# Optimization experiments

Hardware: AMD Instinct MI355X
Metric: run time of the kernel (lower is better)

The kernel has to match this reference:

```python
import jax, jax.numpy as jnp
import numpy as np

N = 8192       # number of points
C = 16         # num_colors (size of color distribution)
DIM = 2        # spatial dim (GeometricLoss(dim=2))


def setup_inputs() -> dict:
    key = jax.random.key(0)
    k1, k2 = jax.random.split(key)
    outputs = jax.random.normal(k1, (N, C), dtype=jnp.float32)
    points = jax.random.normal(k2, (N, DIM), dtype=jnp.float32)
    return {"outputs": outputs, "points": points, "k": 5}


def reference(outputs, points, k):
    # cdist(points, points) via the squared-norm expansion (avoids [N,N,dim] tensor)
    sq = jnp.sum(points * points, axis=1)                      # [N]
    d2 = sq[:, None] + sq[None, :] - 2.0 * (points @ points.T)  # [N,N]
    dist = jnp.sqrt(jnp.maximum(d2, 0.0))
    # k+1 smallest distances per row; drop self (distance 0)
    _, idx = jax.lax.top_k(-dist, k + 1)                        # [N,k+1]
    idx = idx[:, 1:]                                            # [N,k]
    neighbor_outputs = outputs[idx]                             # [N,k,C] gather
    # ||out_i - out_j|| over color dim, mean over all (i, neighbor) pairs
    differences = jnp.linalg.norm(outputs[:, None, :] - neighbor_outputs, axis=2)
    return differences.mean()
```

## Files before the change

### kernel.cpp

```cpp
#include <hip/hip_runtime.h>


static constexpr int NPTS  = 8192;
static constexpr int KNN   = 5;
static constexpr int CH    = 16;
static constexpr int WPB   = 4;
static constexpr int QPW   = 4;
static constexpr int NWAVE = NPTS / QPW;
static constexpr int NBLK  = NWAVE / WPB;
static constexpr int CAP   = 128;
static constexpr int NF4   = NPTS / 2;
static constexpr int BAT   = 4;
static constexpr int NIT   = NF4 / 64;
static constexpr int NB    = NIT / BAT;

__device__ __forceinline__ unsigned long long shfl_xor_u64(unsigned long long v, int m) {
    unsigned int lo = (unsigned int)v;
    unsigned int hi = (unsigned int)(v >> 32);
    lo = __shfl_xor(lo, m, 64);
    hi = __shfl_xor(hi, m, 64);
    return ((unsigned long long)hi << 32) | lo;
}

__global__ __launch_bounds__(256, 4) void knn_loss_kernel(
        const float* __restrict__ outputs,
        const float* __restrict__ points,
        float* __restrict__ partial) {
    const int wave  = threadIdx.x >> 6;
    const int lane  = threadIdx.x & 63;
    const int w     = blockIdx.x * WPB + wave;
    const int qbase = w * QPW;

    const float2* __restrict__ pts2 = (const float2*)points;
    const float4* __restrict__ pts4 = (const float4*)points;
    const float FINF = __int_as_float(0x7f800000);

    float pix[QPW], piy[QPW];
    #pragma unroll
    for (int q = 0; q < QPW; ++q) {
        const float2 p = pts2[qbase + q];
        pix[q] = p.x; piy[q] = p.y;
    }

    float acc[QPW];
    #pragma unroll
    for (int q = 0; q < QPW; ++q) acc[q] = FINF;

    for (int b = 0; b < NB; ++b) {
        float4 p[BAT];
        #pragma unroll
        for (int u = 0; u < BAT; ++u)
            p[u] = pts4[b * (BAT * 64) + u * 64 + lane];
        #pragma unroll
        for (int u = 0; u < BAT; ++u) {
            #pragma unroll
            for (int q = 0; q < QPW; ++q) {
                const float dxa = pix[q] - p[u].x, dya = piy[q] - p[u].y;
                const float dxb = pix[q] - p[u].z, dyb = piy[q] - p[u].w;
                const float d2a = fmaf(dxa, dxa, dya * dya);
                const float d2b = fmaf(dxb, dxb, dyb * dyb);
                acc[q] = fminf(fminf(acc[q], d2a), d2b);
            }
        }
    }

    float v[QPW], T[QPW];
    #pragma unroll
    for (int q = 0; q < QPW; ++q) v[q] = fmaxf(acc[q], 0.0f);
    #pragma unroll
    for (int t = 0; t < KNN + 1; ++t) {
        float m[QPW];
        #pragma unroll
        for (int q = 0; q < QPW; ++q) m[q] = v[q];
        #pragma unroll
        for (int d = 1; d < 64; d <<= 1) {
            #pragma unroll
            for (int q = 0; q < QPW; ++q)
                m[q] = fminf(m[q], __shfl_xor(m[q], d, 64));
        }
        #pragma unroll
        for (int q = 0; q < QPW; ++q) {
            if (v[q] == m[q]) v[q] = FINF;
            T[q] = m[q];
        }
    }

    __shared__ unsigned long long buf[WPB][QPW][CAP];
    __shared__ int cnt[WPB][QPW];
    __shared__ float red[WPB];
    if (lane < QPW) cnt[wave][lane] = 0;
    __syncthreads();

    for (int b = 0; b < NB; ++b) {
        float4 p[BAT];
        #pragma unroll
        for (int u = 0; u < BAT; ++u)
            p[u] = pts4[b * (BAT * 64) + u * 64 + lane];
        #pragma unroll
        for (int u = 0; u < BAT; ++u) {
            const int it = b * (BAT * 64) + u * 64 + lane;
            #pragma unroll
            for (int q = 0; q < QPW; ++q) {
                const float dxa = pix[q] - p[u].x, dya = piy[q] - p[u].y;
                const float dxb = pix[q] - p[u].z, dyb = piy[q] - p[u].w;
                const float d2a = fmaf(dxa, dxa, dya * dya);
                const float d2b = fmaf(dxb, dxb, dyb * dyb);
                if (d2a <= T[q] || d2b <= T[q]) {
                    if (d2a <= T[q]) {
                        const int pos = atomicAdd(&cnt[wave][q], 1);
                        if (pos < CAP)
                            buf[wave][q][pos] =
                                ((unsigned long long)__float_as_uint(fmaxf(d2a, 0.0f)) << 32)
                                | (unsigned int)(2 * it);
                    }
                    if (d2b <= T[q]) {
                        const int pos = atomicAdd(&cnt[wave][q], 1);
                        if (pos < CAP)
                            buf[wave][q][pos] =
                                ((unsigned long long)__float_as_uint(fmaxf(d2b, 0.0f)) << 32)
                                | (unsigned int)(2 * it + 1);
                    }
                }
            }
        }
    }
    __syncthreads();

    const unsigned long long INF64 = ~0ull;
    unsigned int myj = 0;
    int myi = 0, active = 0;
    #pragma unroll
    for (int q = 0; q < QPW; ++q) {
        const int n = min(cnt[wave][q], CAP);
        unsigned long long a  = (lane      < n) ? buf[wave][q][lane]      : INF64;
        unsigned long long b2 = (lane + 64 < n) ? buf[wave][q][lane + 64] : INF64;
        if (b2 < a) { unsigned long long t = a; a = b2; b2 = t; }
        #pragma unroll
        for (int t = 0; t < KNN + 1; ++t) {
            unsigned long long m = a;
            #pragma unroll
            for (int d = 1; d < 64; d <<= 1) {
                const unsigned long long x = shfl_xor_u64(m, d);
                if (x < m) m = x;
            }
            if (a == m) { a = b2; b2 = INF64; }
            if (t >= 1 && lane == q * 8 + t) {
                myj = (unsigned int)m; myi = qbase + q; active = 1;
            }
        }
    }

    float nrm = 0.0f;
    if (active) {
        const float4* oi = (const float4*)(outputs + (size_t)myi * CH);
        const float4* oj = (const float4*)(outputs + (size_t)myj * CH);
        float s = 0.0f;
        #pragma unroll
        for (int c = 0; c < 4; ++c) {
            const float4 x = oi[c], y = oj[c];
            const float dx = x.x - y.x, dy = x.y - y.y;
            const float dz = x.z - y.z, dw = x.w - y.w;
            s += dx * dx + dy * dy + dz * dz + dw * dw;
        }
        nrm = sqrtf(s);
    }
    #pragma unroll
    for (int d = 1; d < 64; d <<= 1) nrm += __shfl_xor(nrm, d, 64);

    if (lane == 0) red[wave] = nrm;
    __syncthreads();
    if (threadIdx.x == 0)
        partial[blockIdx.x] = red[0] + red[1] + red[2] + red[3];
}

__global__ __launch_bounds__(256) void finalize_kernel(
        const float* __restrict__ partial, float* __restrict__ out) {
    double s = 0.0;
    for (int idx = threadIdx.x; idx < NBLK; idx += 256) s += (double)partial[idx];
    #pragma unroll
    for (int d = 1; d < 64; d <<= 1) s += __shfl_xor(s, d, 64);
    __shared__ double lds[4];
    const int wave = threadIdx.x >> 6;
    const int lane = threadIdx.x & 63;
    if (lane == 0) lds[wave] = s;
    __syncthreads();
    if (threadIdx.x == 0)
        out[0] = (float)((lds[0] + lds[1] + lds[2] + lds[3]) /
                         (double)((long long)NPTS * KNN));
}

extern "C" void kernel_launch(void* const* d_in, const int* in_sizes, int n_in,
                              void* d_out, int out_size, void* d_ws, size_t ws_size,
                              hipStream_t stream) {
    const float* outputs = (const float*)d_in[0];
    const float* points  = (const float*)d_in[1];
    float* partial = (float*)d_ws;
    float* out = (float*)d_out;

    knn_loss_kernel<<<NBLK, 256, 0, stream>>>(outputs, points, partial);
    finalize_kernel<<<1, 256, 0, stream>>>(partial, out);
}
```

Baseline: 93.52 us.

## Split each query's candidate scan across a whole block instead of one wave

```diff
diff --git a/kernel.cpp b/kernel.cpp
--- a/kernel.cpp
+++ b/kernel.cpp
@@ -1,18 +1,17 @@
 #include <hip/hip_runtime.h>
 
 
-static constexpr int NPTS  = 8192;
-static constexpr int KNN   = 5;
-static constexpr int CH    = 16;
-static constexpr int WPB   = 4;
-static constexpr int QPW   = 4;
-static constexpr int NWAVE = NPTS / QPW;
-static constexpr int NBLK  = NWAVE / WPB;
-static constexpr int CAP   = 128;
-static constexpr int NF4   = NPTS / 2;
-static constexpr int BAT   = 4;
-static constexpr int NIT   = NF4 / 64;
-static constexpr int NB    = NIT / BAT;
+static constexpr int NPTS    = 8192;
+static constexpr int KNN     = 5;
+static constexpr int CH      = 16;
+static constexpr int QPB     = 4;
+static constexpr int THREADS = 256;
+static constexpr int NBLK    = NPTS / QPB;
+static constexpr int CAP     = 128;
+static constexpr int NF4     = NPTS / 2;
+static constexpr int ITERS   = NF4 / THREADS;
+static constexpr int BAT     = 4;
+static constexpr int NB      = ITERS / BAT;
 
 __device__ __forceinline__ unsigned long long shfl_xor_u64(unsigned long long v, int m) {
     unsigned int lo = (unsigned int)v;
@@ -22,39 +21,39 @@
     return ((unsigned long long)hi << 32) | lo;
 }
 
-__global__ __launch_bounds__(256, 4) void knn_loss_kernel(
+__global__ __launch_bounds__(256, 8) void knn_loss_kernel(
         const float* __restrict__ outputs,
         const float* __restrict__ points,
         float* __restrict__ partial) {
-    const int wave  = threadIdx.x >> 6;
-    const int lane  = threadIdx.x & 63;
-    const int w     = blockIdx.x * WPB + wave;
-    const int qbase = w * QPW;
+    const int tid  = threadIdx.x;
+    const int wave = tid >> 6;
+    const int lane = tid & 63;
+    const int qbase = blockIdx.x * QPB;
 
     const float2* __restrict__ pts2 = (const float2*)points;
     const float4* __restrict__ pts4 = (const float4*)points;
     const float FINF = __int_as_float(0x7f800000);
 
-    float pix[QPW], piy[QPW];
-    #pragma unroll
-    for (int q = 0; q < QPW; ++q) {
+    float pix[QPB], piy[QPB];
+    #pragma unroll
+    for (int q = 0; q < QPB; ++q) {
         const float2 p = pts2[qbase + q];
         pix[q] = p.x; piy[q] = p.y;
     }
 
-    float acc[QPW];
-    #pragma unroll
-    for (int q = 0; q < QPW; ++q) acc[q] = FINF;
+    float acc[QPB];
+    #pragma unroll
+    for (int q = 0; q < QPB; ++q) acc[q] = FINF;
 
     for (int b = 0; b < NB; ++b) {
         float4 p[BAT];
         #pragma unroll
         for (int u = 0; u < BAT; ++u)
-            p[u] = pts4[b * (BAT * 64) + u * 64 + lane];
+            p[u] = pts4[b * (BAT * THREADS) + u * THREADS + tid];
         #pragma unroll
         for (int u = 0; u < BAT; ++u) {
             #pragma unroll
-            for (int q = 0; q < QPW; ++q) {
+            for (int q = 0; q < QPB; ++q) {
                 const float dxa = pix[q] - p[u].x, dya = piy[q] - p[u].y;
                 const float dxb = pix[q] - p[u].z, dyb = piy[q] - p[u].w;
                 const float d2a = fmaf(dxa, dxa, dya * dya);
@@ -64,59 +63,73 @@
         }
     }
 
-    float v[QPW], T[QPW];
-    #pragma unroll
-    for (int q = 0; q < QPW; ++q) v[q] = fmaxf(acc[q], 0.0f);
-    #pragma unroll
-    for (int t = 0; t < KNN + 1; ++t) {
-        float m[QPW];
-        #pragma unroll
-        for (int q = 0; q < QPW; ++q) m[q] = v[q];
-        #pragma unroll
-        for (int d = 1; d < 64; d <<= 1) {
+    __shared__ float thrmin[QPB][THREADS];
+    __shared__ unsigned long long buf[QPB][CAP];
+    __shared__ int cnt[QPB];
+    __shared__ float Ts[QPB];
+    __shared__ float red[QPB];
+
+    #pragma unroll
+    for (int q = 0; q < QPB; ++q)
+        thrmin[q][tid] = fmaxf(acc[q], 0.0f);
+    if (tid < QPB) cnt[tid] = 0;
+    __syncthreads();
+
+    {
+        const float4 tv = ((const float4*)thrmin[wave])[lane];
+        float v = fminf(fminf(tv.x, tv.y), fminf(tv.z, tv.w));
+        float T = 0.0f;
+        #pragma unroll
+        for (int t = 0; t < KNN + 1; ++t) {
+            float m = v;
             #pragma unroll
-            for (int q = 0; q < QPW; ++q)
-                m[q] = fminf(m[q], __shfl_xor(m[q], d, 64));
-        }
-        #pragma unroll
-        for (int q = 0; q < QPW; ++q) {
-            if (v[q] == m[q]) v[q] = FINF;
-            T[q] = m[q];
-        }
-    }
-
-    __shared__ unsigned long long buf[WPB][QPW][CAP];
-    __shared__ int cnt[WPB][QPW];
-    __shared__ float red[WPB];
-    if (lane < QPW) cnt[wave][lane] = 0;
-    __syncthreads();
+            for (int d = 1; d < 64; d <<= 1) m = fminf(m, __shfl_xor(m, d, 64));
+            if (v == m) v = FINF;
+            T = m;
+        }
+        if (lane == 0) Ts[wave] = T;
+    }
+    __syncthreads();
+
+    float Tq[QPB];
+    #pragma unroll
+    for (int q = 0; q < QPB; ++q) Tq[q] = Ts[q];
 
     for (int b = 0; b < NB; ++b) {
         float4 p[BAT];
         #pragma unroll
         for (int u = 0; u < BAT; ++u)
-            p[u] = pts4[b * (BAT * 64) + u * 64 + lane];
+            p[u] = pts4[b * (BAT * THREADS) + u * THREADS + tid];
         #pragma unroll
         for (int u = 0; u < BAT; ++u) {
-            const int it = b * (BAT * 64) + u * 64 + lane;
+            const int it = b * (BAT * THREADS) + u * THREADS + tid;
+            float g = FINF;
             #pragma unroll
-            for (int q = 0; q < QPW; ++q) {
+            for (int q = 0; q < QPB; ++q) {
                 const float dxa = pix[q] - p[u].x, dya = piy[q] - p[u].y;
                 const float dxb = pix[q] - p[u].z, dyb = piy[q] - p[u].w;
                 const float d2a = fmaf(dxa, dxa, dya * dya);
                 const float d2b = fmaf(dxb, dxb, dyb * dyb);
-                if (d2a <= T[q] || d2b <= T[q]) {
-                    if (d2a <= T[q]) {
-                        const int pos = atomicAdd(&cnt[wave][q], 1);
+                g = fminf(g, fminf(d2a, d2b) - Tq[q]);
+            }
+            if (g <= 0.0f) {
+                #pragma unroll
+                for (int q = 0; q < QPB; ++q) {
+                    const float dxa = pix[q] - p[u].x, dya = piy[q] - p[u].y;
+                    const float dxb = pix[q] - p[u].z, dyb = piy[q] - p[u].w;
+                    const float d2a = fmaf(dxa, dxa, dya * dya);
+                    const float d2b = fmaf(dxb, dxb, dyb * dyb);
+                    if (d2a <= Tq[q]) {
+                        const int pos = atomicAdd(&cnt[q], 1);
                         if (pos < CAP)
-                            buf[wave][q][pos] =
+                            buf[q][pos] =
                                 ((unsigned long long)__float_as_uint(fmaxf(d2a, 0.0f)) << 32)
                                 | (unsigned int)(2 * it);
                     }
-                    if (d2b <= T[q]) {
-                        const int pos = atomicAdd(&cnt[wave][q], 1);
+                    if (d2b <= Tq[q]) {
+                        const int pos = atomicAdd(&cnt[q], 1);
                         if (pos < CAP)
-                            buf[wave][q][pos] =
+                            buf[q][pos] =
                                 ((unsigned long long)__float_as_uint(fmaxf(d2b, 0.0f)) << 32)
                                 | (unsigned int)(2 * it + 1);
                     }
@@ -127,32 +140,28 @@
     __syncthreads();
 
     const unsigned long long INF64 = ~0ull;
+    const int n = min(cnt[wave], CAP);
+    unsigned long long a  = (lane      < n) ? buf[wave][lane]      : INF64;
+    unsigned long long b2 = (lane + 64 < n) ? buf[wave][lane + 64] : INF64;
+    if (b2 < a) { unsigned long long t = a; a = b2; b2 = t; }
+
     unsigned int myj = 0;
-    int myi = 0, active = 0;
-    #pragma unroll
-    for (int q = 0; q < QPW; ++q) {
-        const int n = min(cnt[wave][q], CAP);
-        unsigned long long a  = (lane      < n) ? buf[wave][q][lane]      : INF64;
-        unsigned long long b2 = (lane + 64 < n) ? buf[wave][q][lane + 64] : INF64;
-        if (b2 < a) { unsigned long long t = a; a = b2; b2 = t; }
-        #pragma unroll
-        for (int t = 0; t < KNN + 1; ++t) {
-            unsigned long long m = a;
-            #pragma unroll
-            for (int d = 1; d < 64; d <<= 1) {
-                const unsigned long long x = shfl_xor_u64(m, d);
-                if (x < m) m = x;
-            }
-            if (a == m) { a = b2; b2 = INF64; }
-            if (t >= 1 && lane == q * 8 + t) {
-                myj = (unsigned int)m; myi = qbase + q; active = 1;
-            }
-        }
+    int active = 0;
+    #pragma unroll
+    for (int t = 0; t < KNN + 1; ++t) {
+        unsigned long long m = a;
+        #pragma unroll
+        for (int d = 1; d < 64; d <<= 1) {
+            const unsigned long long x = shfl_xor_u64(m, d);
+            if (x < m) m = x;
+        }
+        if (a == m) { a = b2; b2 = INF64; }
+        if (t >= 1 && lane == t) { myj = (unsigned int)m; active = 1; }
     }
 
     float nrm = 0.0f;
     if (active) {
-        const float4* oi = (const float4*)(outputs + (size_t)myi * CH);
+        const float4* oi = (const float4*)(outputs + (size_t)(qbase + wave) * CH);
         const float4* oj = (const float4*)(outputs + (size_t)myj * CH);
         float s = 0.0f;
         #pragma unroll
@@ -169,7 +178,7 @@
 
     if (lane == 0) red[wave] = nrm;
     __syncthreads();
-    if (threadIdx.x == 0)
+    if (tid == 0)
         partial[blockIdx.x] = red[0] + red[1] + red[2] + red[3];
 }
 
@@ -197,6 +206,6 @@
     float* partial = (float*)d_ws;
     float* out = (float*)d_out;
 
-    knn_loss_kernel<<<NBLK, 256, 0, stream>>>(outputs, points, partial);
+    knn_loss_kernel<<<NBLK, THREADS, 0, stream>>>(outputs, points, partial);
     finalize_kernel<<<1, 256, 0, stream>>>(partial, out);
 }
```

After: 84.82 us. 1.1x faster.
